# Performance work log

Hardware: AMD Instinct MI355X
Metric: run time of the kernel (lower is better)

The kernel has to match this reference:

```python
import jax, jax.numpy as jnp
import numpy as np

WORD = 512
ED = 64


def setup_inputs() -> dict:
    key = jax.random.key(0)
    ks = jax.random.split(key, 7)
    x = jax.random.normal(ks[0], (4, 4096, WORD), dtype=jnp.float32)
    # Dense layer params (kernel + bias) for query/key/value projections
    s = 1.0 / np.sqrt(WORD)
    Wq = jax.random.normal(ks[1], (WORD, ED), dtype=jnp.float32) * s
    Wk = jax.random.normal(ks[2], (WORD, ED), dtype=jnp.float32) * s
    Wv = jax.random.normal(ks[3], (WORD, ED), dtype=jnp.float32) * s
    bq = jnp.zeros((ED,), dtype=jnp.float32)
    bk = jnp.zeros((ED,), dtype=jnp.float32)
    bv = jnp.zeros((ED,), dtype=jnp.float32)
    return {"x": x, "Wq": Wq, "bq": bq, "Wk": Wk, "bk": bk, "Wv": Wv, "bv": bv}


def reference(x, Wq, bq, Wk, bk, Wv, bv):
    # Q, K, V: [B, S, ED]
    Q = jnp.einsum('bsw,we->bse', x, Wq) + bq
    K = jnp.einsum('bsw,we->bse', x, Wk) + bk
    V = jnp.einsum('bsw,we->bse', x, Wv) + bv
    scale = 1.0 / jnp.sqrt(jnp.float32(ED))
    score = jnp.einsum('bqe,bke->bqk', Q, K) * scale  # [B, S, S]
    attn = jax.nn.softmax(score, axis=-1)
    Z = jnp.einsum('bqk,bke->bqe', attn, V)  # [B, S, ED]
    return Z
```

## Files before the change

### kernel.cpp

```cpp
#include <hip/hip_runtime.h>
#include <cstdint>


typedef __bf16 bf16x8 __attribute__((ext_vector_type(8)));
typedef float f32x4 __attribute__((ext_vector_type(4)));
typedef float f32x16 __attribute__((ext_vector_type(16)));
typedef int i32x2 __attribute__((ext_vector_type(2)));

#define SCALEQ 0.18033688011112042f

#define WT_OFF 0u
#define Q_OFF  262144u
#define KV_OFF 2359296u
#define L_OFF  6553600u
#define OP_OFF 7077888u

#if defined(__has_builtin)
#if __has_builtin(__builtin_amdgcn_permlane32_swap)
#define HAVE_PLSWAP 1
#endif
#if __has_builtin(__builtin_amdgcn_global_load_lds)
#define HAVE_GLL 1
#endif
#endif
#ifndef HAVE_PLSWAP
#define HAVE_PLSWAP 0
#endif
#ifndef HAVE_GLL
#define HAVE_GLL 0
#endif

__device__ __forceinline__ unsigned short bf16_1(float a) {
  unsigned ua = __builtin_bit_cast(unsigned, a);
  ua += 0x7FFFu + ((ua >> 16) & 1u);
  return (unsigned short)(ua >> 16);
}
__device__ __forceinline__ unsigned pk_bf16(float a, float b) {
  unsigned ua = __builtin_bit_cast(unsigned, a);
  unsigned ub = __builtin_bit_cast(unsigned, b);
  ua += 0x7FFFu + ((ua >> 16) & 1u);
  ub += 0x7FFFu + ((ub >> 16) & 1u);
  return (ua >> 16) | (ub & 0xFFFF0000u);
}
__device__ __forceinline__ unsigned pkru(float lo, float hi) {
  unsigned a = __builtin_bit_cast(unsigned, lo) + 0x8000u;
  unsigned b = __builtin_bit_cast(unsigned, hi) + 0x8000u;
  return __builtin_amdgcn_perm(b, a, 0x07060302u);
}
__device__ __forceinline__ void plswap(unsigned& x, unsigned& y, unsigned hl) {
#if HAVE_PLSWAP
  i32x2 r = __builtin_amdgcn_permlane32_swap((int)x, (int)y, false, false);
  x = (unsigned)r[0];
  y = (unsigned)r[1];
#else
  unsigned xs = (unsigned)__shfl_xor((int)x, 32);
  unsigned ys = (unsigned)__shfl_xor((int)y, 32);
  unsigned nx = hl ? ys : x;
  unsigned ny = hl ? y : xs;
  x = nx;
  y = ny;
#endif
}
#if HAVE_GLL
__device__ __forceinline__ void gll16(const void* g, void* l) {
  __builtin_amdgcn_global_load_lds(
      (const __attribute__((address_space(1))) void*)g,
      (__attribute__((address_space(3))) void*)l, 16, 0, 0);
}
#endif

__global__ __launch_bounds__(256) void prep_w(const float* __restrict__ Wq,
                                              const float* __restrict__ Wk,
                                              const float* __restrict__ Wv,
                                              unsigned short* __restrict__ wt2) {
  unsigned gtid = blockIdx.x * 256u + threadIdx.x;
  unsigned mat = gtid >> 15, rem = gtid & 32767u;
  const float* w = (mat == 0) ? Wq : (mat == 1) ? Wk : Wv;
  float v = w[rem];
  unsigned k = rem >> 6, n = rem & 63u;
  unsigned col = mat * 64u + n;
  unsigned ntg = col >> 4, l15c = col & 15u;
  unsigned kc = k >> 5, quad = (k >> 3) & 3u, j = k & 7u;
  wt2[((ntg * 16u + kc) * 64u + quad * 16u + l15c) * 8u + j] = bf16_1(v);
}

__global__ __launch_bounds__(256, 4) void qkv_proj(
    const float* __restrict__ x, const unsigned short* __restrict__ wt2,
    const float* __restrict__ bq, const float* __restrict__ bk,
    const float* __restrict__ bv, unsigned short* __restrict__ qws,
    unsigned short* __restrict__ kvws) {
  __shared__ __align__(16) char xs[16384];
  __shared__ float biasl[192];
  const unsigned t = threadIdx.x;
  const unsigned row0 = blockIdx.x * 16u;
  const unsigned w = t >> 6, lane = t & 63u, l15 = lane & 15u, quad = lane >> 4;

  if (t < 192u) {
    unsigned mat = t >> 6, n = t & 63u;
    biasl[t] = (mat == 0) ? bq[n] : (mat == 1) ? bk[n] : bv[n];
  }
#pragma unroll
  for (int i = 0; i < 8; i++) {
    unsigned idx4 = t + 256u * (unsigned)i;
    unsigned fidx = idx4 * 4u;
    unsigned row = fidx >> 9, k = fidx & 511u, g = k >> 3;
    float4 f = *(const float4*)(x + row0 * 512u + fidx);
    int2 v = make_int2(pkru(f.x, f.y), pkru(f.z, f.w));
    *(int2*)(xs + row * 1024u + ((g ^ (row & 7u)) << 4) + (k & 7u) * 2u) = v;
  }
  __syncthreads();

  f32x4 acc[3];
#pragma unroll
  for (int i = 0; i < 3; i++) acc[i] = {0.f, 0.f, 0.f, 0.f};
  const unsigned arow = l15;
  const unsigned short* wbase = wt2 + (w * 3u * 1024u + lane) * 8u;

  int4 cur[3], nxt[3];
#pragma unroll
  for (int nt = 0; nt < 3; nt++)
    cur[nt] = *(const int4*)(wbase + (unsigned)nt * 8192u);
  for (unsigned kc = 0; kc < 16u; kc++) {
    if (kc < 15u) {
#pragma unroll
      for (int nt = 0; nt < 3; nt++)
        nxt[nt] = *(const int4*)(wbase + ((unsigned)nt * 16u + kc + 1u) * 512u);
    }
    unsigned ag = kc * 4u + quad;
    int4 av = *(const int4*)(xs + arow * 1024u + ((ag ^ (arow & 7u)) << 4));
    bf16x8 a = __builtin_bit_cast(bf16x8, av);
#pragma unroll
    for (int nt = 0; nt < 3; nt++)
      acc[nt] = __builtin_amdgcn_mfma_f32_16x16x32_bf16(
          a, __builtin_bit_cast(bf16x8, cur[nt]), acc[nt], 0, 0, 0);
#pragma unroll
    for (int nt = 0; nt < 3; nt++) cur[nt] = nxt[nt];
  }
  unsigned sb = row0 + quad * 4u;
#pragma unroll
  for (int nt = 0; nt < 3; nt++) {
    unsigned col = w * 48u + (unsigned)nt * 16u + l15;
    unsigned mat = col >> 6, n = col & 63u;
    float bb = biasl[col];
    if (mat == 0) {
#pragma unroll
      for (int r = 0; r < 4; r++)
        qws[(sb + (unsigned)r) * 64u + n] = bf16_1((acc[nt][r] + bb) * SCALEQ);
    } else if (mat == 1) {
#pragma unroll
      for (int r = 0; r < 4; r++) {
        unsigned s = sb + (unsigned)r;
        unsigned bb2 = s >> 12, tile = (s & 4095u) >> 6, kap = s & 63u;
        kvws[(bb2 * 64u + tile) * 8192u + (n >> 3) * 512u + kap * 8u + (n & 7u)] =
            bf16_1(acc[nt][r] + bb);
      }
    } else {
      unsigned s = sb;
      unsigned bb2 = s >> 12, tile = (s & 4095u) >> 6;
      unsigned kg = (s & 63u) >> 3, j0 = s & 7u;
      int2 pv = make_int2(pk_bf16(acc[nt][0] + bb, acc[nt][1] + bb),
                          pk_bf16(acc[nt][2] + bb, acc[nt][3] + bb));
      *(int2*)(kvws + (bb2 * 64u + tile) * 8192u + (8u + kg) * 512u + n * 8u +
               j0) = pv;
    }
  }
}

__global__ __launch_bounds__(256, 3) void attn(
    const unsigned short* __restrict__ qws,
    const unsigned short* __restrict__ kvws, float* __restrict__ lws,
    unsigned short* __restrict__ opp) {
  __shared__ __align__(16) char sm[34816];
  const unsigned t = threadIdx.x;
  const unsigned w = t >> 6, lane = t & 63u, l31 = lane & 31u, hl = lane >> 5;
  const unsigned bid = blockIdx.x;
  const unsigned ks = bid >> 7;
  const unsigned b = (bid >> 5) & 3u;
  const unsigned qt = bid & 31u;
  const unsigned q0 = qt * 128u + w * 32u;
  const unsigned short* kvb = kvws + (b * 64u + ks * 8u) * 8192u + lane * 8u;

  bf16x8 qf[4];
#pragma unroll
  for (int kq = 0; kq < 4; kq++)
    qf[kq] = __builtin_bit_cast(
        bf16x8, *(const int4*)(qws + (b * 4096u + q0 + l31) * 64u +
                               (unsigned)kq * 16u + hl * 8u));
  f32x16 accO[2];
#pragma unroll
  for (int dh = 0; dh < 2; dh++)
#pragma unroll
    for (int r = 0; r < 16; r++) accO[dh][r] = 0.f;
  float lsum = 0.f;

#if HAVE_GLL
#define STAGE(kt_, bi_)                                                \
  {                                                                    \
    _Pragma("unroll") for (int i = 0; i < 4; i++) {                    \
      unsigned c = (unsigned)i * 4u + w;                               \
      gll16(kvb + (kt_)*8192u + c * 512u, sm + (bi_)*16384u + c * 1024u); \
    }                                                                  \
  }
  STAGE(0u, 0u);
  __syncthreads();
#else
  int4 stg[4];
#define LOADT(kt_)                                                         \
  {                                                                        \
    _Pragma("unroll") for (int i = 0; i < 4; i++) stg[i] =                 \
        *(const int4*)(kvb + (kt_)*8192u + ((unsigned)i * 4u + w) * 512u); \
  }
  LOADT(0u);
  {
#pragma unroll
    for (int i = 0; i < 4; i++)
      *(int4*)(sm + ((unsigned)i * 4u + w) * 1024u + lane * 16u) = stg[i];
  }
  __syncthreads();
#endif

  for (unsigned kt = 0; kt < 8u; kt++) {
    char* kb = sm + (kt & 1u) * 16384u;
    int4 kfr[8], vfr[8];
#pragma unroll
    for (int kq = 0; kq < 4; kq++)
#pragma unroll
      for (int kh = 0; kh < 2; kh++)
        kfr[kq * 2 + kh] = *(const int4*)(
            kb + (((unsigned)kq * 2u + hl) * 64u + (unsigned)kh * 32u + l31) * 16u);
#pragma unroll
    for (int kqg = 0; kqg < 4; kqg++)
#pragma unroll
      for (int dh = 0; dh < 2; dh++)
        vfr[kqg * 2 + dh] = *(const int4*)(
            kb + 8192u +
            (((unsigned)kqg * 2u + hl) * 64u + (unsigned)dh * 32u + l31) * 16u);
#if HAVE_GLL
    if (kt < 7u) STAGE(kt + 1u, (kt + 1u) & 1u);
#else
    if (kt < 7u) LOADT(kt + 1u);
#endif
#pragma unroll
    for (int kh = 0; kh < 2; kh++) {
      f32x16 z;
#pragma unroll
      for (int r = 0; r < 16; r++) z[r] = 0.f;
#pragma unroll
      for (int kq = 0; kq < 4; kq++)
        z = __builtin_amdgcn_mfma_f32_32x32x16_bf16(
            __builtin_bit_cast(bf16x8, kfr[kq * 2 + kh]), qf[kq], z, 0, 0, 0);
      float lp = 0.f;
#pragma unroll
      for (int r = 0; r < 16; r++) {
        z[r] = __builtin_amdgcn_exp2f(z[r]);
        lp += z[r];
      }
      lsum += lp;
      unsigned pk8[8];
#pragma unroll
      for (int c2 = 0; c2 < 4; c2++) {
        pk8[2 * c2] = pkru(z[4 * c2 + 0], z[4 * c2 + 1]);
        pk8[2 * c2 + 1] = pkru(z[4 * c2 + 2], z[4 * c2 + 3]);
      }
#pragma unroll
      for (int kqpl = 0; kqpl < 2; kqpl++) {
        unsigned a0 = pk8[4 * kqpl + 0], a1 = pk8[4 * kqpl + 1];
        unsigned b0 = pk8[4 * kqpl + 2], b1 = pk8[4 * kqpl + 3];
        plswap(a0, b0, hl);
        plswap(a1, b1, hl);
        int4 fr = make_int4((int)a0, (int)a1, (int)b0, (int)b1);
        bf16x8 pf = __builtin_bit_cast(bf16x8, fr);
        unsigned kqg = (unsigned)kh * 2u + (unsigned)kqpl;
#pragma unroll
        for (int dh = 0; dh < 2; dh++)
          accO[dh] = __builtin_amdgcn_mfma_f32_32x32x16_bf16(
              __builtin_bit_cast(bf16x8, vfr[kqg * 2u + (unsigned)dh]), pf,
              accO[dh], 0, 0, 0);
      }
    }
    __syncthreads();
#if !HAVE_GLL
    if (kt < 7u) {
#pragma unroll
      for (int i = 0; i < 4; i++)
        *(int4*)(sm + ((kt + 1u) & 1u) * 16384u +
                 ((unsigned)i * 4u + w) * 1024u + lane * 16u) = stg[i];
      __syncthreads();
    }
#endif
  }
  float lt = lsum + __shfl_xor(lsum, 32);
  if (hl == 0u) lws[ks * 16384u + b * 4096u + q0 + l31] = lt;
  float* sc = (float*)(sm + w * 8704u);
#pragma unroll
  for (int dh = 0; dh < 2; dh++)
#pragma unroll
    for (int r = 0; r < 16; r++) {
      unsigned d = (unsigned)dh * 32u + (unsigned)(r & 3) +
                   8u * (unsigned)(r >> 2) + 4u * hl;
      sc[l31 * 68u + d] = accO[dh][r];
    }
#pragma unroll
  for (int i = 0; i < 4; i++) {
    unsigned ql = (lane >> 3) + (unsigned)i * 8u;
    unsigned d0 = (lane & 7u) * 8u;
    float4 f0 = *(const float4*)(sc + ql * 68u + d0);
    float4 f1 = *(const float4*)(sc + ql * 68u + d0 + 4u);
    int4 pv = make_int4(pkru(f0.x, f0.y), pkru(f0.z, f0.w),
                        pkru(f1.x, f1.y), pkru(f1.z, f1.w));
    *(int4*)(opp + ks * 1048576u + (b * 4096u + q0 + ql) * 64u + d0) = pv;
  }
}

__global__ __launch_bounds__(256) void combine(const unsigned short* __restrict__ opp,
                                               const float* __restrict__ lws,
                                               float* __restrict__ out) {
#pragma unroll
  for (int ii = 0; ii < 2; ii++) {
    unsigned slot = blockIdx.x * 512u + threadIdx.x + 256u * (unsigned)ii;
    unsigned q = slot >> 4, c = (slot & 15u) * 4u;
    float l = 0.f;
#pragma unroll
    for (int s = 0; s < 8; s++) l += lws[(unsigned)s * 16384u + q];
    float inv = 1.0f / l;
    float4 r = make_float4(0.f, 0.f, 0.f, 0.f);
#pragma unroll
    for (int s = 0; s < 8; s++) {
      int2 pv = *(const int2*)(opp + (unsigned)s * 1048576u + q * 64u + c);
      r.x += __builtin_bit_cast(float, (unsigned)pv.x << 16);
      r.y += __builtin_bit_cast(float, (unsigned)pv.x & 0xFFFF0000u);
      r.z += __builtin_bit_cast(float, (unsigned)pv.y << 16);
      r.w += __builtin_bit_cast(float, (unsigned)pv.y & 0xFFFF0000u);
    }
    r.x *= inv; r.y *= inv; r.z *= inv; r.w *= inv;
    *(float4*)(out + q * 64u + c) = r;
  }
}

extern "C" void kernel_launch(void* const* d_in, const int* in_sizes, int n_in,
                              void* d_out, int out_size, void* d_ws,
                              size_t ws_size, hipStream_t stream) {
  const float* x = (const float*)d_in[0];
  const float* Wq = (const float*)d_in[1];
  const float* bq = (const float*)d_in[2];
  const float* Wk = (const float*)d_in[3];
  const float* bk = (const float*)d_in[4];
  const float* Wv = (const float*)d_in[5];
  const float* bv = (const float*)d_in[6];
  char* ws = (char*)d_ws;
  unsigned short* wt2 = (unsigned short*)(ws + WT_OFF);
  unsigned short* qb = (unsigned short*)(ws + Q_OFF);
  unsigned short* kvb = (unsigned short*)(ws + KV_OFF);
  float* lp = (float*)(ws + L_OFF);
  unsigned short* opp = (unsigned short*)(ws + OP_OFF);
  float* outp = (float*)d_out;

  prep_w<<<384, 256, 0, stream>>>(Wq, Wk, Wv, wt2);
  qkv_proj<<<1024, 256, 0, stream>>>(x, wt2, bq, bk, bv, qb, kvb);
  attn<<<1024, 256, 0, stream>>>(qb, kvb, lp, opp);
  combine<<<512, 256, 0, stream>>>(opp, lp, outp);
}
```

Baseline: 119.0 us.

## Load K/V tiles directly into registers with double buffering, halve KV split

The attention kernel no longer stages K/V tiles through shared memory with barriers. Each wave now loads its MFMA fragments straight from global memory into a register double buffer, prefetching the next tile. The KV split drops from 8 to 4 (512 blocks, 16 tiles each), which halves the partial outputs the combine kernel must read. Q is stored in a fragment-major layout so each wave reads it contiguously. The cost is many more registers (launch bounds lowered to 2 blocks per SM), redundant global loads of K/V across the four waves of a block, and fewer blocks to fill the GPU.

```diff
diff --git a/kernel.cpp b/kernel.cpp
--- a/kernel.cpp
+++ b/kernel.cpp
@@ -13,21 +13,15 @@
 #define Q_OFF  262144u
 #define KV_OFF 2359296u
 #define L_OFF  6553600u
-#define OP_OFF 7077888u
+#define OP_OFF 6815744u
 
 #if defined(__has_builtin)
 #if __has_builtin(__builtin_amdgcn_permlane32_swap)
 #define HAVE_PLSWAP 1
 #endif
-#if __has_builtin(__builtin_amdgcn_global_load_lds)
-#define HAVE_GLL 1
-#endif
 #endif
 #ifndef HAVE_PLSWAP
 #define HAVE_PLSWAP 0
-#endif
-#ifndef HAVE_GLL
-#define HAVE_GLL 0
 #endif
 
 __device__ __forceinline__ unsigned short bf16_1(float a) {
@@ -61,13 +55,6 @@
   y = ny;
 #endif
 }
-#if HAVE_GLL
-__device__ __forceinline__ void gll16(const void* g, void* l) {
-  __builtin_amdgcn_global_load_lds(
-      (const __attribute__((address_space(1))) void*)g,
-      (__attribute__((address_space(3))) void*)l, 16, 0, 0);
-}
-#endif
 
 __global__ __launch_bounds__(256) void prep_w(const float* __restrict__ Wq,
                                               const float* __restrict__ Wk,
@@ -87,7 +74,7 @@
 __global__ __launch_bounds__(256, 4) void qkv_proj(
     const float* __restrict__ x, const unsigned short* __restrict__ wt2,
     const float* __restrict__ bq, const float* __restrict__ bk,
-    const float* __restrict__ bv, unsigned short* __restrict__ qws,
+    const float* __restrict__ bv, unsigned short* __restrict__ qfm,
     unsigned short* __restrict__ kvws) {
   __shared__ __align__(16) char xs[16384];
   __shared__ float biasl[192];
@@ -143,9 +130,13 @@
     unsigned mat = col >> 6, n = col & 63u;
     float bb = biasl[col];
     if (mat == 0) {
-#pragma unroll
-      for (int r = 0; r < 4; r++)
-        qws[(sb + (unsigned)r) * 64u + n] = bf16_1((acc[nt][r] + bb) * SCALEQ);
+      unsigned chunk = (n >> 4) * 2u + ((n >> 3) & 1u);
+#pragma unroll
+      for (int r = 0; r < 4; r++) {
+        unsigned q = sb + (unsigned)r;
+        qfm[(q >> 5) * 2048u + chunk * 256u + (q & 31u) * 8u + (n & 7u)] =
+            bf16_1((acc[nt][r] + bb) * SCALEQ);
+      }
     } else if (mat == 1) {
 #pragma unroll
       for (int r = 0; r < 4; r++) {
@@ -166,8 +157,8 @@
   }
 }
 
-__global__ __launch_bounds__(256, 3) void attn(
-    const unsigned short* __restrict__ qws,
+__global__ __launch_bounds__(256, 2) void attn(
+    const unsigned short* __restrict__ qfm,
     const unsigned short* __restrict__ kvws, float* __restrict__ lws,
     unsigned short* __restrict__ opp) {
   __shared__ __align__(16) char sm[34816];
@@ -178,14 +169,14 @@
   const unsigned b = (bid >> 5) & 3u;
   const unsigned qt = bid & 31u;
   const unsigned q0 = qt * 128u + w * 32u;
-  const unsigned short* kvb = kvws + (b * 64u + ks * 8u) * 8192u + lane * 8u;
-
+
+  const unsigned qtile = b * 128u + qt * 4u + w;
   bf16x8 qf[4];
 #pragma unroll
   for (int kq = 0; kq < 4; kq++)
     qf[kq] = __builtin_bit_cast(
-        bf16x8, *(const int4*)(qws + (b * 4096u + q0 + l31) * 64u +
-                               (unsigned)kq * 16u + hl * 8u));
+        bf16x8, *(const int4*)(qfm + qtile * 2048u +
+                               ((unsigned)kq * 2u + hl) * 256u + l31 * 8u));
   f32x16 accO[2];
 #pragma unroll
   for (int dh = 0; dh < 2; dh++)
@@ -193,53 +184,34 @@
     for (int r = 0; r < 16; r++) accO[dh][r] = 0.f;
   float lsum = 0.f;
 
-#if HAVE_GLL
-#define STAGE(kt_, bi_)                                                \
-  {                                                                    \
-    _Pragma("unroll") for (int i = 0; i < 4; i++) {                    \
-      unsigned c = (unsigned)i * 4u + w;                               \
-      gll16(kvb + (kt_)*8192u + c * 512u, sm + (bi_)*16384u + c * 1024u); \
-    }                                                                  \
-  }
-  STAGE(0u, 0u);
-  __syncthreads();
-#else
-  int4 stg[4];
-#define LOADT(kt_)                                                         \
-  {                                                                        \
-    _Pragma("unroll") for (int i = 0; i < 4; i++) stg[i] =                 \
-        *(const int4*)(kvb + (kt_)*8192u + ((unsigned)i * 4u + w) * 512u); \
-  }
-  LOADT(0u);
-  {
-#pragma unroll
-    for (int i = 0; i < 4; i++)
-      *(int4*)(sm + ((unsigned)i * 4u + w) * 1024u + lane * 16u) = stg[i];
-  }
-  __syncthreads();
-#endif
-
-  for (unsigned kt = 0; kt < 8u; kt++) {
-    char* kb = sm + (kt & 1u) * 16384u;
-    int4 kfr[8], vfr[8];
-#pragma unroll
-    for (int kq = 0; kq < 4; kq++)
-#pragma unroll
-      for (int kh = 0; kh < 2; kh++)
-        kfr[kq * 2 + kh] = *(const int4*)(
-            kb + (((unsigned)kq * 2u + hl) * 64u + (unsigned)kh * 32u + l31) * 16u);
-#pragma unroll
-    for (int kqg = 0; kqg < 4; kqg++)
-#pragma unroll
-      for (int dh = 0; dh < 2; dh++)
-        vfr[kqg * 2 + dh] = *(const int4*)(
-            kb + 8192u +
-            (((unsigned)kqg * 2u + hl) * 64u + (unsigned)dh * 32u + l31) * 16u);
-#if HAVE_GLL
-    if (kt < 7u) STAGE(kt + 1u, (kt + 1u) & 1u);
-#else
-    if (kt < 7u) LOADT(kt + 1u);
-#endif
+  const unsigned short* kvt = kvws + (b * 64u + ks * 16u) * 8192u;
+  const unsigned loff = hl * 512u + l31 * 8u;
+
+  int4 bufK[2][8], bufV[2][8];
+#define LOADKV(kt_, KB, VB)                                                   \
+  do {                                                                        \
+    const unsigned short* p = kvt + (kt_)*8192u + loff;                       \
+    _Pragma("unroll") for (int i = 0; i < 8; i++) {                           \
+      KB[i] = *(const int4*)(p + (unsigned)(i >> 1) * 1024u +                 \
+                             (unsigned)(i & 1) * 256u);                       \
+      VB[i] = *(const int4*)(p + 4096u + (unsigned)(i >> 1) * 1024u +         \
+                             (unsigned)(i & 1) * 256u);                       \
+    }                                                                         \
+  } while (0)
+  LOADKV(0u, bufK[0], bufV[0]);
+
+#pragma unroll 2
+  for (unsigned kt = 0; kt < 16u; kt++) {
+    const unsigned cb = kt & 1u;
+    if (kt < 15u) {
+      if (cb == 0u) {
+        LOADKV(kt + 1u, bufK[1], bufV[1]);
+      } else {
+        LOADKV(kt + 1u, bufK[0], bufV[0]);
+      }
+    }
+    const int4* kfr = bufK[cb];
+    const int4* vfr = bufV[cb];
 #pragma unroll
     for (int kh = 0; kh < 2; kh++) {
       f32x16 z;
@@ -278,16 +250,6 @@
               accO[dh], 0, 0, 0);
       }
     }
-    __syncthreads();
-#if !HAVE_GLL
-    if (kt < 7u) {
-#pragma unroll
-      for (int i = 0; i < 4; i++)
-        *(int4*)(sm + ((kt + 1u) & 1u) * 16384u +
-                 ((unsigned)i * 4u + w) * 1024u + lane * 16u) = stg[i];
-      __syncthreads();
-    }
-#endif
   }
   float lt = lsum + __shfl_xor(lsum, 32);
   if (hl == 0u) lws[ks * 16384u + b * 4096u + q0 + l31] = lt;
@@ -321,11 +283,11 @@
     unsigned q = slot >> 4, c = (slot & 15u) * 4u;
     float l = 0.f;
 #pragma unroll
-    for (int s = 0; s < 8; s++) l += lws[(unsigned)s * 16384u + q];
+    for (int s = 0; s < 4; s++) l += lws[(unsigned)s * 16384u + q];
     float inv = 1.0f / l;
     float4 r = make_float4(0.f, 0.f, 0.f, 0.f);
 #pragma unroll
-    for (int s = 0; s < 8; s++) {
+    for (int s = 0; s < 4; s++) {
       int2 pv = *(const int2*)(opp + (unsigned)s * 1048576u + q * 64u + c);
       r.x += __builtin_bit_cast(float, (unsigned)pv.x << 16);
       r.y += __builtin_bit_cast(float, (unsigned)pv.x & 0xFFFF0000u);
@@ -357,6 +319,6 @@
 
   prep_w<<<384, 256, 0, stream>>>(Wq, Wk, Wv, wt2);
   qkv_proj<<<1024, 256, 0, stream>>>(x, wt2, bq, bk, bv, qb, kvb);
-  attn<<<1024, 256, 0, stream>>>(qb, kvb, lp, opp);
+  attn<<<512, 256, 0, stream>>>(qb, kvb, lp, opp);
   combine<<<512, 256, 0, stream>>>(opp, lp, outp);
 }
```

After: 120.4 us. Within noise of the previous version (+1.2%).
